# Optimization experiments

Measured on AMD Instinct MI355X. Metric: run time of the kernel, lower is better.

The kernel has to match this reference:

```python
import jax, jax.numpy as jnp
import numpy as np

V, E, H, ENC = 10000, 512, 512, 2048
B, T, P = 64, 64, 196


def setup_inputs() -> dict:
    key = jax.random.key(0)
    ks = jax.random.split(key, 12)
    s = 0.02
    return {
        "encoder_out": jax.random.normal(ks[0], (B, P, ENC), jnp.float32),
        "targets": jax.random.randint(ks[1], (B, T), 0, V),
        "embedding": jax.random.normal(ks[2], (V, E), jnp.float32) * s,
        "W_ih": jax.random.normal(ks[3], (4 * H, E), jnp.float32) * s,
        "W_hh": jax.random.normal(ks[4], (4 * H, H), jnp.float32) * s,
        "b_ih": jnp.zeros((4 * H,), jnp.float32),
        "b_hh": jnp.zeros((4 * H,), jnp.float32),
        "Wh": jax.random.normal(ks[5], (H, ENC), jnp.float32) * s,
        "bh": jnp.zeros((H,), jnp.float32),
        "Wc": jax.random.normal(ks[6], (H, ENC), jnp.float32) * s,
        "bc": jnp.zeros((H,), jnp.float32),
        "Wout": jax.random.normal(ks[7], (V, H), jnp.float32) * s,
        "bout": jnp.zeros((V,), jnp.float32),
    }


def reference(encoder_out, targets, embedding, W_ih, W_hh, b_ih, b_hh, Wh, bh, Wc, bc, Wout, bout):
    # init hidden state from mean-pooled encoder features
    mean_enc = encoder_out.mean(axis=1)                      # [B, ENC]
    h0 = jnp.tanh(mean_enc @ Wh.T + bh)                      # [B, H]
    c0 = jnp.tanh(mean_enc @ Wc.T + bc)                      # [B, H]

    Bsz, Tlen = targets.shape
    # teacher forcing (ratio=1.0): input at step t is targets[:, t-1]
    emb = embedding[targets[:, :-1]]                         # [B, T-1, E]
    # precompute input-dependent gate pre-activations (dropout = eval identity)
    xg = jnp.einsum('bte,ge->btg', emb, W_ih) + b_ih + b_hh  # [B, T-1, 4H]

    def step(carry, x):
        h, c = carry
        gates = x + h @ W_hh.T                               # [B, 4H]
        i, f, g, o = jnp.split(gates, 4, axis=-1)
        i = jax.nn.sigmoid(i)
        f = jax.nn.sigmoid(f)
        g = jnp.tanh(g)
        o = jax.nn.sigmoid(o)
        c = f * c + i * g
        h = o * jnp.tanh(c)
        out = h @ Wout.T + bout                              # [B, V]
        return (h, c), out

    _, outs = jax.lax.scan(step, (h0, c0), jnp.swapaxes(xg, 0, 1))
    outs = jnp.swapaxes(outs, 0, 1)                          # [B, T-1, V]
    zeros0 = jnp.zeros((Bsz, 1, outs.shape[-1]), outs.dtype)  # step 0 untouched
    return jnp.concatenate([zeros0, outs], axis=1)           # [B, T, V]
```

## Files before the change

kernel.cpp:

```cpp
#include <hip/hip_runtime.h>

typedef __bf16 bf16x8 __attribute__((ext_vector_type(8)));
typedef float f32x4 __attribute__((ext_vector_type(4)));

static __device__ __forceinline__ unsigned short f2bf(float f) {
    unsigned u = __builtin_bit_cast(unsigned, f);
    unsigned r = u + 0x7fffu + ((u >> 16) & 1u);
    return (unsigned short)(r >> 16);
}

#define GLD_LDS16(g, l) __builtin_amdgcn_global_load_lds( \
    (const __attribute__((address_space(1))) unsigned int*)(const void*)(g), \
    (__attribute__((address_space(3))) unsigned int*)(void*)(l), 16, 0, 0)

__global__ __launch_bounds__(256) void k_prep(
    const float* Wih, const float* Whh, const float* Wh, const float* Wc,
    const float* Wout, const float* emb, const int* targets,
    unsigned short* Wih_b, unsigned short* Whh_b, unsigned short* Wh_b,
    unsigned short* Wc_b, unsigned short* Wout_b, unsigned short* Aemb,
    float* out, int* ctrs, float* ps)
{
    const long N0 = 1048576, N1 = 1048576, N2 = 1048576, N3 = 1048576;
    const long N4 = 5120000, N5 = 2064384, N6 = 640000, N7 = 256, N8 = 65536;
    const long total = N0 + N1 + N2 + N3 + N4 + N5 + N6 + N7 + N8;
    const long stride = (long)gridDim.x * blockDim.x;
    for (long i = (long)blockIdx.x * blockDim.x + threadIdx.x; i < total; i += stride) {
        long j = i;
        if (j < N0) { Wih_b[j] = f2bf(Wih[j]); continue; } j -= N0;
        if (j < N1) { Whh_b[j] = f2bf(Whh[j]); continue; } j -= N1;
        if (j < N2) { Wh_b[j]  = f2bf(Wh[j]);  continue; } j -= N2;
        if (j < N3) { Wc_b[j]  = f2bf(Wc[j]);  continue; } j -= N3;
        if (j < N4) { Wout_b[j] = f2bf(Wout[j]); continue; } j -= N4;
        if (j < N5) {
            long m = j >> 9; int k = (int)(j & 511);
            int b = (int)(m / 63), t = (int)(m - (long)b * 63);
            int row = targets[b * 64 + t];
            Aemb[j] = f2bf(emb[(long)row * 512 + k]);
            continue;
        } j -= N5;
        if (j < N6) {
            long b = j / 10000, v = j - b * 10000;
            out[b * 640000 + v] = 0.f;
            continue;
        } j -= N6;
        if (j < N7) { ctrs[j] = 0; continue; } j -= N7;
        ps[j] = 0.f;
    }
}

__global__ __launch_bounds__(128) void k_mean(const float* enc, unsigned short* mean_b)
{
    int b = blockIdx.y;
    int c = blockIdx.x * 128 + threadIdx.x;
    const float* base = enc + (long)b * 196 * 2048 + c;
    float s0 = 0.f, s1 = 0.f, s2 = 0.f, s3 = 0.f;
    for (int p = 0; p < 196; p += 4) {
        s0 += base[(long)(p + 0) * 2048];
        s1 += base[(long)(p + 1) * 2048];
        s2 += base[(long)(p + 2) * 2048];
        s3 += base[(long)(p + 3) * 2048];
    }
    mean_b[(long)b * 2048 + c] = f2bf((s0 + s1 + s2 + s3) * (1.f / 196.f));
}

__global__ __launch_bounds__(256) void k_h0c0(
    const unsigned short* A, const unsigned short* Whb, const unsigned short* Wcb,
    float* ps)
{
    __shared__ unsigned short As[64 * 40];
    __shared__ unsigned short Bs[64 * 40];
    const int tid = threadIdx.x;
    const int n0 = blockIdx.x * 64;
    const int kc = blockIdx.y * 16;
    const int w = tid >> 6, lane = tid & 63, quad = lane >> 4, l16 = lane & 15;
    const int r = tid >> 2, seg = tid & 3;
    f32x4 acc[4];
#pragma unroll
    for (int i = 0; i < 4; i++) acc[i] = (f32x4){0.f, 0.f, 0.f, 0.f};

    for (int kb = kc; kb < kc + 16; kb++) {
        int k0 = kb * 32;
        *(uint4*)&As[r * 40 + seg * 8] = *(const uint4*)&A[(long)r * 2048 + k0 + seg * 8];
        int ngr = n0 + r;
        const unsigned short* bsrc = (ngr < 512) ? (Whb + (long)ngr * 2048)
                                                 : (Wcb + (long)(ngr - 512) * 2048);
        *(uint4*)&Bs[r * 40 + seg * 8] = *(const uint4*)&bsrc[k0 + seg * 8];
        __syncthreads();
        bf16x8 bfr = *(const bf16x8*)&Bs[(16 * w + l16) * 40 + quad * 8];
#pragma unroll
        for (int mt = 0; mt < 4; mt++) {
            bf16x8 af = *(const bf16x8*)&As[(mt * 16 + l16) * 40 + quad * 8];
            acc[mt] = __builtin_amdgcn_mfma_f32_16x16x32_bf16(af, bfr, acc[mt], 0, 0, 0);
        }
        __syncthreads();
    }
    int ng = n0 + 16 * w + l16;
#pragma unroll
    for (int mt = 0; mt < 4; mt++) {
#pragma unroll
        for (int rr = 0; rr < 4; rr++) {
            int m = mt * 16 + quad * 4 + rr;
            atomicAdd(&ps[(long)m * 1024 + ng], acc[mt][rr]);
        }
    }
}

__global__ __launch_bounds__(256) void k_fin(
    const float* ps, const float* bh, const float* bc,
    unsigned short* Hbuf, float* c0buf)
{
    int i = blockIdx.x * 256 + threadIdx.x;
    int m = i >> 10, ng = i & 1023;
    int j = ng & 511;
    float bias = (ng < 512) ? bh[j] : bc[j];
    float v = tanhf(ps[i] + bias);
    if (ng < 512) Hbuf[(long)m * 512 + j] = f2bf(v);
    else          c0buf[(long)m * 512 + j] = v;
}

__global__ __launch_bounds__(256) void k_xg(
    const unsigned short* A, const unsigned short* Bw,
    const float* bih, const float* bhh, float* xg)
{
    __shared__ unsigned short As[64 * 40];
    __shared__ unsigned short Bs[64 * 40];
    const int tid = threadIdx.x;
    const int n0 = blockIdx.x * 64, m0 = blockIdx.y * 64;
    const int w = tid >> 6, lane = tid & 63, quad = lane >> 4, l16 = lane & 15;
    const int r = tid >> 2, seg = tid & 3;
    f32x4 acc[4];
#pragma unroll
    for (int i = 0; i < 4; i++) acc[i] = (f32x4){0.f, 0.f, 0.f, 0.f};

    for (int kb = 0; kb < 16; kb++) {
        int k0 = kb * 32;
        *(uint4*)&As[r * 40 + seg * 8] = *(const uint4*)&A[(long)(m0 + r) * 512 + k0 + seg * 8];
        *(uint4*)&Bs[r * 40 + seg * 8] = *(const uint4*)&Bw[(long)(n0 + r) * 512 + k0 + seg * 8];
        __syncthreads();
        bf16x8 bfr = *(const bf16x8*)&Bs[(16 * w + l16) * 40 + quad * 8];
#pragma unroll
        for (int mt = 0; mt < 4; mt++) {
            bf16x8 af = *(const bf16x8*)&As[(mt * 16 + l16) * 40 + quad * 8];
            acc[mt] = __builtin_amdgcn_mfma_f32_16x16x32_bf16(af, bfr, acc[mt], 0, 0, 0);
        }
        __syncthreads();
    }
    int ng = n0 + 16 * w + l16;
    float bias = bih[ng] + bhh[ng];
#pragma unroll
    for (int mt = 0; mt < 4; mt++) {
#pragma unroll
        for (int rr = 0; rr < 4; rr++) {
            int m = m0 + mt * 16 + quad * 4 + rr;
            xg[(long)m * 2048 + ng] = acc[mt][rr] + bias;
        }
    }
}

__global__ __launch_bounds__(256, 1) void k_scan(
    const unsigned short* Whh_b, const float* xg, const float* c0buf,
    unsigned short* Hbuf, int* ctrs)
{
    __shared__ unsigned short Wlds[128 * 520];
    __shared__ unsigned short hs[16 * 520];
    __shared__ float gs[16 * 133];
    const int tid = threadIdx.x;
    const int gid = blockIdx.x;
    const int b0 = (gid & 3) * 16;
    const int j0 = (gid >> 2) * 32;
    const int w = tid >> 6, lane = tid & 63, quad = lane >> 4, l16 = lane & 15;
    const int m = tid >> 4, u0 = (tid & 15) * 2;

    for (int nrel = w; nrel < 128; nrel += 4) {
        int q = nrel >> 5, u = nrel & 31;
        *(uint4*)&Wlds[nrel * 520 + lane * 8] =
            *(const uint4*)&Whh_b[(long)(q * 512 + j0 + u) * 512 + lane * 8];
    }
    float2 cr = *(const float2*)&c0buf[(long)(b0 + m) * 512 + j0 + u0];
    float c0v = cr.x, c1v = cr.y;
    int* ctr = ctrs + (gid & 3) * 64;
    __syncthreads();

    for (int s = 1; s < 64; s++) {
        const float* xb = xg + ((long)(b0 + m) * 63 + (s - 1)) * 2048 + j0 + u0;
        float2 xv0 = *(const float2*)(xb + 0);
        float2 xv1 = *(const float2*)(xb + 512);
        float2 xv2 = *(const float2*)(xb + 1024);
        float2 xv3 = *(const float2*)(xb + 1536);

        const unsigned* hsrc = (const unsigned*)(Hbuf + ((long)(s - 1) * 64 + b0) * 512);
        unsigned hv[16];
#pragma unroll
        for (int j = 0; j < 16; j++)
            hv[j] = __hip_atomic_load(hsrc + j * 256 + tid, __ATOMIC_RELAXED,
                                      __HIP_MEMORY_SCOPE_AGENT);
#pragma unroll
        for (int j = 0; j < 16; j++)
            *(unsigned*)&hs[j * 520 + tid * 2] = hv[j];
        __syncthreads();

        f32x4 acc0 = (f32x4){0.f, 0.f, 0.f, 0.f};
        f32x4 acc1 = (f32x4){0.f, 0.f, 0.f, 0.f};
#pragma unroll
        for (int kk = 0; kk < 16; kk++) {
            bf16x8 a  = *(const bf16x8*)&hs[l16 * 520 + kk * 32 + quad * 8];
            bf16x8 bA = *(const bf16x8*)&Wlds[(32 * w + l16) * 520 + kk * 32 + quad * 8];
            bf16x8 bB = *(const bf16x8*)&Wlds[(32 * w + 16 + l16) * 520 + kk * 32 + quad * 8];
            acc0 = __builtin_amdgcn_mfma_f32_16x16x32_bf16(a, bA, acc0, 0, 0, 0);
            acc1 = __builtin_amdgcn_mfma_f32_16x16x32_bf16(a, bB, acc1, 0, 0, 0);
        }
#pragma unroll
        for (int rr = 0; rr < 4; rr++) {
            gs[(quad * 4 + rr) * 133 + 32 * w + l16] = acc0[rr];
            gs[(quad * 4 + rr) * 133 + 32 * w + 16 + l16] = acc1[rr];
        }
        __syncthreads();

        float gi0 = gs[m * 133 + u0]          + xv0.x;
        float gi1 = gs[m * 133 + u0 + 1]      + xv0.y;
        float gf0 = gs[m * 133 + 32 + u0]     + xv1.x;
        float gf1 = gs[m * 133 + 33 + u0]     + xv1.y;
        float gg0 = gs[m * 133 + 64 + u0]     + xv2.x;
        float gg1 = gs[m * 133 + 65 + u0]     + xv2.y;
        float go0 = gs[m * 133 + 96 + u0]     + xv3.x;
        float go1 = gs[m * 133 + 97 + u0]     + xv3.y;
        float cn0 = (1.f / (1.f + __expf(-gf0))) * c0v + (1.f / (1.f + __expf(-gi0))) * tanhf(gg0);
        float cn1 = (1.f / (1.f + __expf(-gf1))) * c1v + (1.f / (1.f + __expf(-gi1))) * tanhf(gg1);
        c0v = cn0; c1v = cn1;
        float h0v = (1.f / (1.f + __expf(-go0))) * tanhf(cn0);
        float h1v = (1.f / (1.f + __expf(-go1))) * tanhf(cn1);
        unsigned hp = (unsigned)f2bf(h0v) | ((unsigned)f2bf(h1v) << 16);
        __hip_atomic_store((unsigned*)(Hbuf + ((long)s * 64 + b0 + m) * 512 + j0 + u0), hp,
                           __ATOMIC_RELAXED, __HIP_MEMORY_SCOPE_AGENT);

        if (s < 63) {
            __syncthreads();
            if (tid == 0) {
                __hip_atomic_fetch_add(ctr, 1, __ATOMIC_RELEASE, __HIP_MEMORY_SCOPE_AGENT);
                int target = s * 16;
                while (__hip_atomic_load(ctr, __ATOMIC_RELAXED, __HIP_MEMORY_SCOPE_AGENT) < target) {}
            }
            __syncthreads();
        }
    }
}

__global__ __launch_bounds__(256) void k_out(
    const unsigned short* A, const unsigned short* Wob, const float* bout, float* out)
{
    __shared__ unsigned short As[128 * 32];
    __shared__ unsigned short Bs[128 * 32];
    const int tid = threadIdx.x;
    const int n0 = blockIdx.x * 128, m0 = blockIdx.y * 128;
    const int w = tid >> 6, lane = tid & 63, quad = lane >> 4, l16 = lane & 15;
    const int wm = w >> 1, wn = w & 1;
    const int gr = lane >> 2, gc = (lane & 3) * 8;

    f32x4 acc[4][4];
#pragma unroll
    for (int i = 0; i < 4; i++)
#pragma unroll
        for (int j = 0; j < 4; j++) acc[i][j] = (f32x4){0.f, 0.f, 0.f, 0.f};

    for (int kb = 0; kb < 16; kb++) {
        int k0 = kb * 32;
#pragma unroll
        for (int p = 0; p < 2; p++) {
            int rowa = m0 + p * 64 + w * 16 + gr;
            GLD_LDS16(A + (long)rowa * 512 + k0 + gc, As + (p * 64 + w * 16) * 32);
            int rowb = n0 + p * 64 + w * 16 + gr;
            GLD_LDS16(Wob + (long)rowb * 512 + k0 + gc, Bs + (p * 64 + w * 16) * 32);
        }
        __syncthreads();
        bf16x8 af[4], bf[4];
#pragma unroll
        for (int mt = 0; mt < 4; mt++)
            af[mt] = *(const bf16x8*)&As[(wm * 64 + mt * 16 + l16) * 32 + quad * 8];
#pragma unroll
        for (int nt = 0; nt < 4; nt++)
            bf[nt] = *(const bf16x8*)&Bs[(wn * 64 + nt * 16 + l16) * 32 + quad * 8];
#pragma unroll
        for (int mt = 0; mt < 4; mt++)
#pragma unroll
            for (int nt = 0; nt < 4; nt++)
                acc[mt][nt] = __builtin_amdgcn_mfma_f32_16x16x32_bf16(af[mt], bf[nt], acc[mt][nt], 0, 0, 0);
        __syncthreads();
    }
#pragma unroll
    for (int nt = 0; nt < 4; nt++) {
        int n = n0 + wn * 64 + nt * 16 + l16;
        if (n >= 10000) continue;
        float bias = bout[n];
#pragma unroll
        for (int mt = 0; mt < 4; mt++) {
#pragma unroll
            for (int rr = 0; rr < 4; rr++) {
                int r = m0 + wm * 64 + mt * 16 + quad * 4 + rr;
                if (r < 4032) {
                    int s = (r >> 6) + 1, b = r & 63;
                    out[((long)b * 64 + s) * 10000 + n] = acc[mt][nt][rr] + bias;
                }
            }
        }
    }
}

extern "C" void kernel_launch(void* const* d_in, const int* in_sizes, int n_in,
                              void* d_out, int out_size, void* d_ws, size_t ws_size,
                              hipStream_t stream)
{
    const float* enc     = (const float*)d_in[0];
    const int*   targets = (const int*)d_in[1];
    const float* emb     = (const float*)d_in[2];
    const float* Wih     = (const float*)d_in[3];
    const float* Whh     = (const float*)d_in[4];
    const float* bih     = (const float*)d_in[5];
    const float* bhh     = (const float*)d_in[6];
    const float* Wh      = (const float*)d_in[7];
    const float* bh      = (const float*)d_in[8];
    const float* Wc      = (const float*)d_in[9];
    const float* bc      = (const float*)d_in[10];
    const float* Wout    = (const float*)d_in[11];
    const float* bout    = (const float*)d_in[12];
    float* out = (float*)d_out;

    char* ws = (char*)d_ws;
    size_t off = 0;
    auto alloc = [&](size_t bytes) {
        void* p = ws + off;
        off = (off + bytes + 255) & ~(size_t)255;
        return p;
    };
    unsigned short* mean_b = (unsigned short*)alloc((size_t)64 * 2048 * 2);
    unsigned short* Wih_b  = (unsigned short*)alloc((size_t)2048 * 512 * 2);
    unsigned short* Whh_b  = (unsigned short*)alloc((size_t)2048 * 512 * 2);
    unsigned short* Wh_b   = (unsigned short*)alloc((size_t)512 * 2048 * 2);
    unsigned short* Wc_b   = (unsigned short*)alloc((size_t)512 * 2048 * 2);
    unsigned short* Wout_b = (unsigned short*)alloc((size_t)10000 * 512 * 2);
    unsigned short* Aemb   = (unsigned short*)alloc((size_t)4032 * 512 * 2);
    float*          xg     = (float*)alloc((size_t)4032 * 2048 * 4);
    unsigned short* Hbuf   = (unsigned short*)alloc((size_t)64 * 64 * 512 * 2);
    float*          c0buf  = (float*)alloc((size_t)64 * 512 * 4);
    int*            ctrs   = (int*)alloc(256 * 4);
    float*          ps     = (float*)alloc((size_t)64 * 1024 * 4);

    k_prep<<<4096, 256, 0, stream>>>(Wih, Whh, Wh, Wc, Wout, emb, targets,
                                     Wih_b, Whh_b, Wh_b, Wc_b, Wout_b, Aemb, out, ctrs, ps);
    k_mean<<<dim3(16, 64), 128, 0, stream>>>(enc, mean_b);
    k_h0c0<<<dim3(16, 4), 256, 0, stream>>>(mean_b, Wh_b, Wc_b, ps);
    k_fin<<<256, 256, 0, stream>>>(ps, bh, bc, Hbuf, c0buf);
    k_xg<<<dim3(32, 63), 256, 0, stream>>>(Aemb, Wih_b, bih, bhh, xg);
    k_scan<<<64, 256, 0, stream>>>(Whh_b, xg, c0buf, Hbuf, ctrs);
    k_out<<<dim3(79, 32), 256, 0, stream>>>(Hbuf + 64 * 512, Wout_b, bout, out);
}
```

Before: 653.3 us.

## Replace scan grid barrier with per-wave flags, retile xg GEMM to 128x128

The recurrent scan kernel drops its counter-based global barrier. Each wave now publishes a per-slice flag after storing its part of h, and consumers poll the flag array with a wave-wide any before loading h straight into MFMA operand registers, which removes the LDS staging and two block barriers per step. The gate buffer is double-buffered so one sync per step is enough. The xg input-projection GEMM moves to 128x128 tiles with direct global-to-LDS loads, and the buffers are padded for the out-of-range tail rows. Sigmoid and tanh use exp-based fast approximations, which slightly change numerics, and flag-based ordering relies on relaxed atomics plus vmcnt waits, so there is a memory-ordering risk.

```diff
diff --git a/kernel.cpp b/kernel.cpp
--- a/kernel.cpp
+++ b/kernel.cpp
@@ -7,6 +7,13 @@
     unsigned u = __builtin_bit_cast(unsigned, f);
     unsigned r = u + 0x7fffu + ((u >> 16) & 1u);
     return (unsigned short)(r >> 16);
+}
+
+static __device__ __forceinline__ float fsig(float x) {
+    return 1.f / (1.f + __expf(-x));
+}
+static __device__ __forceinline__ float ftanh(float x) {
+    return 1.f - 2.f / (1.f + __expf(2.f * x));
 }
 
 #define GLD_LDS16(g, l) __builtin_amdgcn_global_load_lds( \
@@ -122,52 +129,71 @@
     const unsigned short* A, const unsigned short* Bw,
     const float* bih, const float* bhh, float* xg)
 {
-    __shared__ unsigned short As[64 * 40];
-    __shared__ unsigned short Bs[64 * 40];
+    __shared__ unsigned short As[128 * 32];
+    __shared__ unsigned short Bs[128 * 32];
     const int tid = threadIdx.x;
-    const int n0 = blockIdx.x * 64, m0 = blockIdx.y * 64;
+    const int n0 = blockIdx.x * 128, m0 = blockIdx.y * 128;
     const int w = tid >> 6, lane = tid & 63, quad = lane >> 4, l16 = lane & 15;
-    const int r = tid >> 2, seg = tid & 3;
-    f32x4 acc[4];
-#pragma unroll
-    for (int i = 0; i < 4; i++) acc[i] = (f32x4){0.f, 0.f, 0.f, 0.f};
+    const int wm = w >> 1, wn = w & 1;
+    const int gr = lane >> 2, gc = (lane & 3) * 8;
+
+    f32x4 acc[4][4];
+#pragma unroll
+    for (int i = 0; i < 4; i++)
+#pragma unroll
+        for (int j = 0; j < 4; j++) acc[i][j] = (f32x4){0.f, 0.f, 0.f, 0.f};
 
     for (int kb = 0; kb < 16; kb++) {
         int k0 = kb * 32;
-        *(uint4*)&As[r * 40 + seg * 8] = *(const uint4*)&A[(long)(m0 + r) * 512 + k0 + seg * 8];
-        *(uint4*)&Bs[r * 40 + seg * 8] = *(const uint4*)&Bw[(long)(n0 + r) * 512 + k0 + seg * 8];
-        __syncthreads();
-        bf16x8 bfr = *(const bf16x8*)&Bs[(16 * w + l16) * 40 + quad * 8];
+#pragma unroll
+        for (int p = 0; p < 2; p++) {
+            int rowa = m0 + p * 64 + w * 16 + gr;
+            GLD_LDS16(A + (long)rowa * 512 + k0 + gc, As + (p * 64 + w * 16) * 32);
+            int rowb = n0 + p * 64 + w * 16 + gr;
+            GLD_LDS16(Bw + (long)rowb * 512 + k0 + gc, Bs + (p * 64 + w * 16) * 32);
+        }
+        __syncthreads();
+        bf16x8 af[4], bf[4];
+#pragma unroll
+        for (int mt = 0; mt < 4; mt++)
+            af[mt] = *(const bf16x8*)&As[(wm * 64 + mt * 16 + l16) * 32 + quad * 8];
+#pragma unroll
+        for (int nt = 0; nt < 4; nt++)
+            bf[nt] = *(const bf16x8*)&Bs[(wn * 64 + nt * 16 + l16) * 32 + quad * 8];
+#pragma unroll
+        for (int mt = 0; mt < 4; mt++)
+#pragma unroll
+            for (int nt = 0; nt < 4; nt++)
+                acc[mt][nt] = __builtin_amdgcn_mfma_f32_16x16x32_bf16(af[mt], bf[nt], acc[mt][nt], 0, 0, 0);
+        __syncthreads();
+    }
+#pragma unroll
+    for (int nt = 0; nt < 4; nt++) {
+        int n = n0 + wn * 64 + nt * 16 + l16;
+        float bias = bih[n] + bhh[n];
 #pragma unroll
         for (int mt = 0; mt < 4; mt++) {
-            bf16x8 af = *(const bf16x8*)&As[(mt * 16 + l16) * 40 + quad * 8];
-            acc[mt] = __builtin_amdgcn_mfma_f32_16x16x32_bf16(af, bfr, acc[mt], 0, 0, 0);
-        }
-        __syncthreads();
-    }
-    int ng = n0 + 16 * w + l16;
-    float bias = bih[ng] + bhh[ng];
-#pragma unroll
-    for (int mt = 0; mt < 4; mt++) {
-#pragma unroll
-        for (int rr = 0; rr < 4; rr++) {
-            int m = m0 + mt * 16 + quad * 4 + rr;
-            xg[(long)m * 2048 + ng] = acc[mt][rr] + bias;
+#pragma unroll
+            for (int rr = 0; rr < 4; rr++) {
+                int r = m0 + wm * 64 + mt * 16 + quad * 4 + rr;
+                if (r < 4032) xg[(long)r * 2048 + n] = acc[mt][nt][rr] + bias;
+            }
         }
     }
 }
 
 __global__ __launch_bounds__(256, 1) void k_scan(
     const unsigned short* Whh_b, const float* xg, const float* c0buf,
-    unsigned short* Hbuf, int* ctrs)
+    unsigned short* Hbuf, int* flags)
 {
     __shared__ unsigned short Wlds[128 * 520];
-    __shared__ unsigned short hs[16 * 520];
-    __shared__ float gs[16 * 133];
+    __shared__ float gs[2][16 * 133];
     const int tid = threadIdx.x;
     const int gid = blockIdx.x;
-    const int b0 = (gid & 3) * 16;
-    const int j0 = (gid >> 2) * 32;
+    const int grp = gid & 3;
+    const int b0 = grp * 16;
+    const int slice = gid >> 2;
+    const int j0 = slice * 32;
     const int w = tid >> 6, lane = tid & 63, quad = lane >> 4, l16 = lane & 15;
     const int m = tid >> 4, u0 = (tid & 15) * 2;
 
@@ -178,7 +204,7 @@
     }
     float2 cr = *(const float2*)&c0buf[(long)(b0 + m) * 512 + j0 + u0];
     float c0v = cr.x, c1v = cr.y;
-    int* ctr = ctrs + (gid & 3) * 64;
+    int* myfl = flags + grp * 64;
     __syncthreads();
 
     for (int s = 1; s < 64; s++) {
@@ -188,59 +214,70 @@
         float2 xv2 = *(const float2*)(xb + 1024);
         float2 xv3 = *(const float2*)(xb + 1536);
 
-        const unsigned* hsrc = (const unsigned*)(Hbuf + ((long)(s - 1) * 64 + b0) * 512);
-        unsigned hv[16];
-#pragma unroll
-        for (int j = 0; j < 16; j++)
-            hv[j] = __hip_atomic_load(hsrc + j * 256 + tid, __ATOMIC_RELAXED,
+        {
+            const int target = s - 1;
+            int f;
+            do {
+                f = __hip_atomic_load(myfl + lane, __ATOMIC_RELAXED,
                                       __HIP_MEMORY_SCOPE_AGENT);
-#pragma unroll
-        for (int j = 0; j < 16; j++)
-            *(unsigned*)&hs[j * 520 + tid * 2] = hv[j];
-        __syncthreads();
+            } while (__any(f < target));
+        }
+        asm volatile("" ::: "memory");
+
+        const unsigned long long* hsrc = (const unsigned long long*)Hbuf
+            + ((long)(s - 1) * 64 + b0 + l16) * 128 + quad * 2;
+        unsigned long long hv[32];
+#pragma unroll
+        for (int kk = 0; kk < 16; kk++) {
+            hv[kk * 2 + 0] = __hip_atomic_load(hsrc + kk * 8 + 0, __ATOMIC_RELAXED,
+                                               __HIP_MEMORY_SCOPE_AGENT);
+            hv[kk * 2 + 1] = __hip_atomic_load(hsrc + kk * 8 + 1, __ATOMIC_RELAXED,
+                                               __HIP_MEMORY_SCOPE_AGENT);
+        }
 
         f32x4 acc0 = (f32x4){0.f, 0.f, 0.f, 0.f};
         f32x4 acc1 = (f32x4){0.f, 0.f, 0.f, 0.f};
 #pragma unroll
         for (int kk = 0; kk < 16; kk++) {
-            bf16x8 a  = *(const bf16x8*)&hs[l16 * 520 + kk * 32 + quad * 8];
+            union { unsigned long long u[2]; bf16x8 v; } a;
+            a.u[0] = hv[kk * 2 + 0];
+            a.u[1] = hv[kk * 2 + 1];
             bf16x8 bA = *(const bf16x8*)&Wlds[(32 * w + l16) * 520 + kk * 32 + quad * 8];
             bf16x8 bB = *(const bf16x8*)&Wlds[(32 * w + 16 + l16) * 520 + kk * 32 + quad * 8];
-            acc0 = __builtin_amdgcn_mfma_f32_16x16x32_bf16(a, bA, acc0, 0, 0, 0);
-            acc1 = __builtin_amdgcn_mfma_f32_16x16x32_bf16(a, bB, acc1, 0, 0, 0);
-        }
+            acc0 = __builtin_amdgcn_mfma_f32_16x16x32_bf16(a.v, bA, acc0, 0, 0, 0);
+            acc1 = __builtin_amdgcn_mfma_f32_16x16x32_bf16(a.v, bB, acc1, 0, 0, 0);
+        }
+
+        float* g = gs[s & 1];
 #pragma unroll
         for (int rr = 0; rr < 4; rr++) {
-            gs[(quad * 4 + rr) * 133 + 32 * w + l16] = acc0[rr];
-            gs[(quad * 4 + rr) * 133 + 32 * w + 16 + l16] = acc1[rr];
-        }
-        __syncthreads();
-
-        float gi0 = gs[m * 133 + u0]          + xv0.x;
-        float gi1 = gs[m * 133 + u0 + 1]      + xv0.y;
-        float gf0 = gs[m * 133 + 32 + u0]     + xv1.x;
-        float gf1 = gs[m * 133 + 33 + u0]     + xv1.y;
-        float gg0 = gs[m * 133 + 64 + u0]     + xv2.x;
-        float gg1 = gs[m * 133 + 65 + u0]     + xv2.y;
-        float go0 = gs[m * 133 + 96 + u0]     + xv3.x;
-        float go1 = gs[m * 133 + 97 + u0]     + xv3.y;
-        float cn0 = (1.f / (1.f + __expf(-gf0))) * c0v + (1.f / (1.f + __expf(-gi0))) * tanhf(gg0);
-        float cn1 = (1.f / (1.f + __expf(-gf1))) * c1v + (1.f / (1.f + __expf(-gi1))) * tanhf(gg1);
+            g[(quad * 4 + rr) * 133 + 32 * w + l16]      = acc0[rr];
+            g[(quad * 4 + rr) * 133 + 32 * w + 16 + l16] = acc1[rr];
+        }
+        __syncthreads();
+
+        float gi0 = g[m * 133 + u0]      + xv0.x;
+        float gi1 = g[m * 133 + u0 + 1]  + xv0.y;
+        float gf0 = g[m * 133 + 32 + u0] + xv1.x;
+        float gf1 = g[m * 133 + 33 + u0] + xv1.y;
+        float gg0 = g[m * 133 + 64 + u0] + xv2.x;
+        float gg1 = g[m * 133 + 65 + u0] + xv2.y;
+        float go0 = g[m * 133 + 96 + u0] + xv3.x;
+        float go1 = g[m * 133 + 97 + u0] + xv3.y;
+        float cn0 = fsig(gf0) * c0v + fsig(gi0) * ftanh(gg0);
+        float cn1 = fsig(gf1) * c1v + fsig(gi1) * ftanh(gg1);
         c0v = cn0; c1v = cn1;
-        float h0v = (1.f / (1.f + __expf(-go0))) * tanhf(cn0);
-        float h1v = (1.f / (1.f + __expf(-go1))) * tanhf(cn1);
+        float h0v = fsig(go0) * ftanh(cn0);
+        float h1v = fsig(go1) * ftanh(cn1);
         unsigned hp = (unsigned)f2bf(h0v) | ((unsigned)f2bf(h1v) << 16);
         __hip_atomic_store((unsigned*)(Hbuf + ((long)s * 64 + b0 + m) * 512 + j0 + u0), hp,
                            __ATOMIC_RELAXED, __HIP_MEMORY_SCOPE_AGENT);
 
         if (s < 63) {
-            __syncthreads();
-            if (tid == 0) {
-                __hip_atomic_fetch_add(ctr, 1, __ATOMIC_RELEASE, __HIP_MEMORY_SCOPE_AGENT);
-                int target = s * 16;
-                while (__hip_atomic_load(ctr, __ATOMIC_RELAXED, __HIP_MEMORY_SCOPE_AGENT) < target) {}
-            }
-            __syncthreads();
+            asm volatile("s_waitcnt vmcnt(0)" ::: "memory");
+            if (lane == 0)
+                __hip_atomic_store(myfl + slice * 4 + w, s, __ATOMIC_RELAXED,
+                                   __HIP_MEMORY_SCOPE_AGENT);
         }
     }
 }
@@ -337,9 +374,9 @@
     unsigned short* Wh_b   = (unsigned short*)alloc((size_t)512 * 2048 * 2);
     unsigned short* Wc_b   = (unsigned short*)alloc((size_t)512 * 2048 * 2);
     unsigned short* Wout_b = (unsigned short*)alloc((size_t)10000 * 512 * 2);
-    unsigned short* Aemb   = (unsigned short*)alloc((size_t)4032 * 512 * 2);
+    unsigned short* Aemb   = (unsigned short*)alloc((size_t)(4032 + 64) * 512 * 2);
     float*          xg     = (float*)alloc((size_t)4032 * 2048 * 4);
-    unsigned short* Hbuf   = (unsigned short*)alloc((size_t)64 * 64 * 512 * 2);
+    unsigned short* Hbuf   = (unsigned short*)alloc((size_t)(64 * 64 + 64) * 512 * 2);
     float*          c0buf  = (float*)alloc((size_t)64 * 512 * 4);
     int*            ctrs   = (int*)alloc(256 * 4);
     float*          ps     = (float*)alloc((size_t)64 * 1024 * 4);
@@ -349,7 +386,7 @@
     k_mean<<<dim3(16, 64), 128, 0, stream>>>(enc, mean_b);
     k_h0c0<<<dim3(16, 4), 256, 0, stream>>>(mean_b, Wh_b, Wc_b, ps);
     k_fin<<<256, 256, 0, stream>>>(ps, bh, bc, Hbuf, c0buf);
-    k_xg<<<dim3(32, 63), 256, 0, stream>>>(Aemb, Wih_b, bih, bhh, xg);
+    k_xg<<<dim3(16, 32), 256, 0, stream>>>(Aemb, Wih_b, bih, bhh, xg);
     k_scan<<<64, 256, 0, stream>>>(Whh_b, xg, c0buf, Hbuf, ctrs);
     k_out<<<dim3(79, 32), 256, 0, stream>>>(Hbuf + 64 * 512, Wout_b, bout, out);
 }
```

After: 887.9 us. 1.36x slower.
